# Kernel optimization log

Hardware: AMD Instinct MI355X
Metric: run time of the kernel (lower is better)

## Reference

```python
import jax, jax.numpy as jnp
import numpy as np

B, S, E, H = 4, 2048, 1024, 8
D = E // H  # head_dim = 128


def setup_inputs() -> dict:
    key = jax.random.key(0)
    ks = jax.random.split(key, 7)
    scale = 1.0 / np.sqrt(D)
    return {
        "sequences": jax.random.normal(ks[0], (B, S, E), dtype=jnp.float32),
        # per-head Linear weights, torch layout [out, in] stacked over heads
        "Wq": jax.random.normal(ks[1], (H, D, D), dtype=jnp.float32) * scale,
        "Wk": jax.random.normal(ks[2], (H, D, D), dtype=jnp.float32) * scale,
        "Wv": jax.random.normal(ks[3], (H, D, D), dtype=jnp.float32) * scale,
        "bq": jax.random.normal(ks[4], (H, D), dtype=jnp.float32) * scale,
        "bk": jax.random.normal(ks[5], (H, D), dtype=jnp.float32) * scale,
        "bv": jax.random.normal(ks[6], (H, D), dtype=jnp.float32) * scale,
    }


def reference(sequences, Wq, Wk, Wv, bq, bk, bv):
    # split feature dim into heads: [B,S,H,D]
    xh = sequences.reshape(B, S, H, D)
    # torch Linear: y = x @ W.T + b  ->  contract input dim d with W[h, o, d]
    q = jnp.einsum("bshd,hod->bsho", xh, Wq) + bq
    k = jnp.einsum("bshd,hod->bsho", xh, Wk) + bk
    v = jnp.einsum("bshd,hod->bsho", xh, Wv) + bv
    # NOTE: original scales by 1/sqrt(num_heads), not 1/sqrt(head_dim)
    scores = jnp.einsum("bshd,bthd->bhst", q, k) / jnp.sqrt(jnp.float32(H))
    attn = jax.nn.softmax(scores, axis=-1)  # [B,H,S,S]
    out = jnp.einsum("bhst,bthd->bshd", attn, v)
    # hstack over heads == reshape back to [B,S,E]
    return out.reshape(B, S, E)
```

## Files before the change

kernel.cpp:

```cpp
#include <hip/hip_runtime.h>
#include <hip/hip_bf16.h>

#define B_ 4
#define S_ 2048
#define E_ 1024
#define H_ 8
#define D_ 128

using f16x8 = __attribute__((ext_vector_type(8))) _Float16;
using f32x4 = __attribute__((ext_vector_type(4))) float;

__device__ __forceinline__ ushort f2h_bits(float f) {
    union { _Float16 h; ushort u; } cv; cv.h = (_Float16)f; return cv.u;
}
__device__ __forceinline__ f16x8 pack8(const float* __restrict__ p) {
    float4 f0 = *(const float4*)p;
    float4 f1 = *(const float4*)(p + 4);
    f16x8 r;
    r[0] = (_Float16)f0.x; r[1] = (_Float16)f0.y;
    r[2] = (_Float16)f0.z; r[3] = (_Float16)f0.w;
    r[4] = (_Float16)f1.x; r[5] = (_Float16)f1.y;
    r[6] = (_Float16)f1.z; r[7] = (_Float16)f1.w;
    return r;
}

__global__ __launch_bounds__(256) void kv_proj(
    const float* __restrict__ seq,
    const float* __restrict__ Wk, const float* __restrict__ Wv,
    const float* __restrict__ bk, const float* __restrict__ bv,
    ushort* __restrict__ ko, ushort* __restrict__ vo)
{
    constexpr int TS = 136;
    __shared__ ushort Tk[128 * TS];
    __shared__ ushort Tv[128 * TS];
    const int m0 = blockIdx.x * 128, h = blockIdx.y;
    const int tid = threadIdx.x, lane = tid & 63, w = tid >> 6;
    const int l16 = lane & 15, quad = lane >> 4;

    f16x8 a[2][4];
    #pragma unroll
    for (int mt = 0; mt < 2; ++mt)
        #pragma unroll
        for (int ks = 0; ks < 4; ++ks)
            a[mt][ks] = pack8(&seq[(size_t)(m0 + w * 32 + mt * 16 + l16) * E_
                                   + h * D_ + ks * 32 + quad * 8]);

    {
        const float* W = Wk + (size_t)h * D_ * D_;
        f32x4 acc[2][8];
        #pragma unroll
        for (int mt = 0; mt < 2; ++mt)
            #pragma unroll
            for (int nt = 0; nt < 8; ++nt) { f32x4 z = {0.f,0.f,0.f,0.f}; acc[mt][nt] = z; }
        #pragma unroll
        for (int ks = 0; ks < 4; ++ks)
            #pragma unroll
            for (int nt = 0; nt < 8; ++nt) {
                f16x8 bfr = pack8(&W[(size_t)(nt * 16 + l16) * D_ + ks * 32 + quad * 8]);
                #pragma unroll
                for (int mt = 0; mt < 2; ++mt)
                    acc[mt][nt] = __builtin_amdgcn_mfma_f32_16x16x32_f16(
                        a[mt][ks], bfr, acc[mt][nt], 0, 0, 0);
            }
        #pragma unroll
        for (int nt = 0; nt < 8; ++nt) {
            int o = nt * 16 + l16;
            float bias = bk[h * D_ + o];
            #pragma unroll
            for (int mt = 0; mt < 2; ++mt)
                #pragma unroll
                for (int r = 0; r < 4; ++r) {
                    int row = w * 32 + mt * 16 + quad * 4 + r;
                    Tk[row * TS + (o ^ (quad << 3))] = f2h_bits(acc[mt][nt][r] + bias);
                }
        }
    }
    {
        const float* W = Wv + (size_t)h * D_ * D_;
        f32x4 acc[2][8];
        #pragma unroll
        for (int mt = 0; mt < 2; ++mt)
            #pragma unroll
            for (int nt = 0; nt < 8; ++nt) { f32x4 z = {0.f,0.f,0.f,0.f}; acc[mt][nt] = z; }
        #pragma unroll
        for (int ks = 0; ks < 4; ++ks)
            #pragma unroll
            for (int nt = 0; nt < 8; ++nt) {
                f16x8 bfr = pack8(&W[(size_t)(nt * 16 + l16) * D_ + ks * 32 + quad * 8]);
                #pragma unroll
                for (int mt = 0; mt < 2; ++mt)
                    acc[mt][nt] = __builtin_amdgcn_mfma_f32_16x16x32_f16(
                        a[mt][ks], bfr, acc[mt][nt], 0, 0, 0);
            }
        #pragma unroll
        for (int nt = 0; nt < 8; ++nt) {
            int o = nt * 16 + l16;
            float bias = bv[h * D_ + o];
            #pragma unroll
            for (int mt = 0; mt < 2; ++mt)
                #pragma unroll
                for (int r = 0; r < 4; ++r) {
                    int row = w * 32 + mt * 16 + quad * 4 + r;
                    Tv[o * TS + row] = f2h_bits(acc[mt][nt][r] + bias);
                }
        }
    }
    __syncthreads();

    #pragma unroll
    for (int i = 0; i < 8; ++i) {
        int idx = tid + i * 256;
        int row = idx >> 4, c8 = (idx & 15) * 8;
        uint4 dk = *(uint4*)&Tk[row * TS + (c8 ^ (((row >> 2) & 3) << 3))];
        int m = m0 + row, bi = m >> 11, s = m & (S_ - 1);
        *(uint4*)&ko[(((size_t)bi * H_ + h) * S_ + s) * D_ + c8] = dk;
        uint4 dv = *(uint4*)&Tv[row * TS + c8];
        int mg = m0 + c8, bv_i = mg >> 11, s0 = mg & (S_ - 1);
        *(uint4*)&vo[(((size_t)bv_i * H_ + h) * D_ + row) * S_ + s0] = dv;
    }
}

__global__ __launch_bounds__(256) void attn(
    const float* __restrict__ seq, const float* __restrict__ Wq,
    const float* __restrict__ bq,
    const ushort* __restrict__ kg, const ushort* __restrict__ vtg,
    float* __restrict__ out)
{
    constexpr int KS = 136;
    constexpr int VS = 136;
    __shared__ alignas(16) ushort smem[128 * KS + 128 * VS];
    ushort* const Klds = smem;
    ushort* const Vt   = smem + 128 * KS;

    const int m0 = blockIdx.x * 128;
    const int h = blockIdx.y, bi = blockIdx.z;
    const int bh = bi * H_ + h;
    const int tid = threadIdx.x, lane = tid & 63, w = tid >> 6;
    const int l16 = lane & 15, quad = lane >> 4;
    const size_t baseK = (size_t)bh * S_ * D_;
    const size_t baseV = (size_t)bh * D_ * S_;
    const float qscale = 0.35355339059327373f * 1.4426950408889634f;
    const int qq_r = (l16 >> 2) & 3;

    {
        f16x8 xa[2][4];
        #pragma unroll
        for (int mt = 0; mt < 2; ++mt)
            #pragma unroll
            for (int ks = 0; ks < 4; ++ks)
                xa[mt][ks] = pack8(&seq[((size_t)bi * S_ + m0 + w * 32 + mt * 16 + l16) * E_
                                        + h * D_ + ks * 32 + quad * 8]);
        f32x4 qacc[2][8];
        #pragma unroll
        for (int mt = 0; mt < 2; ++mt)
            #pragma unroll
            for (int nt = 0; nt < 8; ++nt) { f32x4 z = {0.f,0.f,0.f,0.f}; qacc[mt][nt] = z; }
        const float* W = Wq + (size_t)h * D_ * D_;
        #pragma unroll
        for (int ks = 0; ks < 4; ++ks)
            #pragma unroll
            for (int nt = 0; nt < 8; ++nt) {
                f16x8 bfr = pack8(&W[(size_t)(nt * 16 + l16) * D_ + ks * 32 + quad * 8]);
                #pragma unroll
                for (int mt = 0; mt < 2; ++mt)
                    qacc[mt][nt] = __builtin_amdgcn_mfma_f32_16x16x32_f16(
                        xa[mt][ks], bfr, qacc[mt][nt], 0, 0, 0);
            }
        #pragma unroll
        for (int nt = 0; nt < 8; ++nt) {
            int o = nt * 16 + l16;
            float bias = bq[h * D_ + o];
            #pragma unroll
            for (int mt = 0; mt < 2; ++mt)
                #pragma unroll
                for (int r = 0; r < 4; ++r) {
                    int row = w * 32 + mt * 16 + quad * 4 + r;
                    Klds[row * KS + (o ^ (quad << 3))] =
                        f2h_bits((qacc[mt][nt][r] + bias) * qscale);
                }
        }
    }
    __syncthreads();

    f16x8 qf[2][4];
    #pragma unroll
    for (int mt = 0; mt < 2; ++mt)
        #pragma unroll
        for (int ks = 0; ks < 4; ++ks)
            qf[mt][ks] = *(const f16x8*)&Klds[(w * 32 + mt * 16 + l16) * KS
                                              + ks * 32 + ((quad ^ qq_r) << 3)];

    f32x4 o_acc[2][8];
    #pragma unroll
    for (int mt = 0; mt < 2; ++mt)
        #pragma unroll
        for (int nt = 0; nt < 8; ++nt) { f32x4 z = {0.f,0.f,0.f,0.f}; o_acc[mt][nt] = z; }
    float m_prev[2] = {-1e30f, -1e30f};
    float l_lane[2] = {0.f, 0.f};

    for (int j = 0; j < S_ / 128; ++j) {
        const int n0 = j * 128;
        __syncthreads();
        #pragma unroll
        for (int i = 0; i < 8; ++i) {
            int idx = tid + i * 256;
            int r = idx >> 4, c8 = (idx & 15) * 8;
            *(uint4*)&Klds[r * KS + c8] =
                *(const uint4*)&kg[baseK + (size_t)(n0 + r) * D_ + c8];
        }
        #pragma unroll
        for (int i = 0; i < 8; ++i) {
            int idx = tid + i * 256;
            int d = idx >> 4, c8 = (idx & 15) * 8;
            *(uint4*)&Vt[d * VS + c8] =
                *(const uint4*)&vtg[baseV + (size_t)d * S_ + n0 + c8];
        }
        __syncthreads();

        f32x4 sacc[2][8];
        #pragma unroll
        for (int mt = 0; mt < 2; ++mt)
            #pragma unroll
            for (int nt = 0; nt < 8; ++nt) { f32x4 z = {0.f,0.f,0.f,0.f}; sacc[mt][nt] = z; }
        __builtin_amdgcn_s_setprio(1);
        #pragma unroll
        for (int ks = 0; ks < 4; ++ks)
            #pragma unroll
            for (int nt = 0; nt < 8; ++nt) {
                f16x8 kf = *(const f16x8*)&Klds[(nt * 16 + l16) * KS + ks * 32 + quad * 8];
                #pragma unroll
                for (int mt = 0; mt < 2; ++mt)
                    sacc[mt][nt] = __builtin_amdgcn_mfma_f32_16x16x32_f16(
                        kf, qf[mt][ks], sacc[mt][nt], 0, 0, 0);
            }
        __builtin_amdgcn_s_setprio(0);

        uint2 pkw[2][8];
        #pragma unroll
        for (int mt = 0; mt < 2; ++mt) {
            float mx4[8];
            #pragma unroll
            for (int nt = 0; nt < 8; ++nt)
                mx4[nt] = fmaxf(fmaxf(sacc[mt][nt][0], sacc[mt][nt][1]),
                                fmaxf(sacc[mt][nt][2], sacc[mt][nt][3]));
            float mx = fmaxf(fmaxf(fmaxf(mx4[0], mx4[1]), fmaxf(mx4[2], mx4[3])),
                             fmaxf(fmaxf(mx4[4], mx4[5]), fmaxf(mx4[6], mx4[7])));
            mx = fmaxf(mx, __shfl_xor(mx, 16));
            mx = fmaxf(mx, __shfl_xor(mx, 32));
            if (__any(mx > m_prev[mt] + 8.0f)) {
                float mnew  = fmaxf(m_prev[mt], mx);
                float alpha = exp2f(m_prev[mt] - mnew);
                #pragma unroll
                for (int nt = 0; nt < 8; ++nt)
                    #pragma unroll
                    for (int r = 0; r < 4; ++r) o_acc[mt][nt][r] *= alpha;
                l_lane[mt] *= alpha;
                m_prev[mt] = mnew;
            }
            #pragma unroll
            for (int nt = 0; nt < 8; ++nt) {
                float e0 = exp2f(sacc[mt][nt][0] - m_prev[mt]);
                float e1 = exp2f(sacc[mt][nt][1] - m_prev[mt]);
                float e2 = exp2f(sacc[mt][nt][2] - m_prev[mt]);
                float e3 = exp2f(sacc[mt][nt][3] - m_prev[mt]);
                auto p01 = __builtin_amdgcn_cvt_pkrtz(e0, e1);
                auto p23 = __builtin_amdgcn_cvt_pkrtz(e2, e3);
                l_lane[mt] += (float)p01[0] + (float)p01[1]
                            + (float)p23[0] + (float)p23[1];
                pkw[mt][nt] = make_uint2(__builtin_bit_cast(uint, p01),
                                         __builtin_bit_cast(uint, p23));
            }
        }

        __syncthreads();
        #pragma unroll
        for (int mt = 0; mt < 2; ++mt) {
            const int qrow = w * 32 + mt * 16 + l16;
            #pragma unroll
            for (int nt = 0; nt < 8; ++nt)
                *(uint2*)&Klds[qrow * KS + nt * 16 + quad * 4] = pkw[mt][nt];
        }

        __builtin_amdgcn_s_setprio(1);
        #pragma unroll
        for (int ks = 0; ks < 4; ++ks) {
            f16x8 pb[2];
            #pragma unroll
            for (int mt = 0; mt < 2; ++mt)
                pb[mt] = *(const f16x8*)&Klds[(w * 32 + mt * 16 + l16) * KS
                                              + ks * 32 + quad * 8];
            #pragma unroll
            for (int nt = 0; nt < 8; ++nt) {
                f16x8 vf = *(const f16x8*)&Vt[(nt * 16 + l16) * VS + ks * 32 + quad * 8];
                #pragma unroll
                for (int mt = 0; mt < 2; ++mt)
                    o_acc[mt][nt] = __builtin_amdgcn_mfma_f32_16x16x32_f16(
                        vf, pb[mt], o_acc[mt][nt], 0, 0, 0);
            }
        }
        __builtin_amdgcn_s_setprio(0);
    }

    #pragma unroll
    for (int mt = 0; mt < 2; ++mt) {
        float l = l_lane[mt];
        l += __shfl_xor(l, 16);
        l += __shfl_xor(l, 32);
        float rinv = 1.0f / l;
        const int q = m0 + w * 32 + mt * 16 + l16;
        #pragma unroll
        for (int nt = 0; nt < 8; ++nt) {
            float4 o;
            o.x = o_acc[mt][nt][0] * rinv;
            o.y = o_acc[mt][nt][1] * rinv;
            o.z = o_acc[mt][nt][2] * rinv;
            o.w = o_acc[mt][nt][3] * rinv;
            *(float4*)&out[((size_t)bi * S_ + q) * E_ + h * D_ + nt * 16 + quad * 4] = o;
        }
    }
}

extern "C" void kernel_launch(void* const* d_in, const int* in_sizes, int n_in,
                              void* d_out, int out_size, void* d_ws, size_t ws_size,
                              hipStream_t stream) {
    const float* seq = (const float*)d_in[0];
    const float* Wq  = (const float*)d_in[1];
    const float* Wk  = (const float*)d_in[2];
    const float* Wv  = (const float*)d_in[3];
    const float* bq  = (const float*)d_in[4];
    const float* bk  = (const float*)d_in[5];
    const float* bv  = (const float*)d_in[6];

    const size_t per = (size_t)B_ * H_ * S_ * D_;
    if (ws_size < 2 * per * sizeof(ushort)) return;
    ushort* kws  = (ushort*)d_ws;
    ushort* vtws = kws + per;

    kv_proj<<<dim3(B_ * S_ / 128, H_), 256, 0, stream>>>(
        seq, Wk, Wv, bk, bv, kws, vtws);
    attn<<<dim3(S_ / 128, H_, B_), 256, 0, stream>>>(
        seq, Wq, bq, kws, vtws, (float*)d_out);
}
```

Measured before the change: 293.8 us.

## Double-buffer K/V with direct global-to-LDS loads and 512-thread attention blocks

The attention kernel moves to 8 waves per block, with each wave owning 16 query rows instead of 32. K and V tiles are now fetched with global_load_lds DMA into double-buffered LDS, so the next tile's load overlaps the current tile's compute, and each loop iteration needs only one barrier. An XOR swizzle, applied in kv_proj's stores and matched in the attention reads, replaces the padded row strides to avoid bank conflicts. The trade-off is heavy LDS use (about 160 KB), which likely limits residency to one block per CU where two could run before.

```diff
diff --git a/kernel.cpp b/kernel.cpp
--- a/kernel.cpp
+++ b/kernel.cpp
@@ -22,6 +22,12 @@
     r[4] = (_Float16)f1.x; r[5] = (_Float16)f1.y;
     r[6] = (_Float16)f1.z; r[7] = (_Float16)f1.w;
     return r;
+}
+
+__device__ __forceinline__ void gll16(const ushort* g, ushort* l) {
+    __builtin_amdgcn_global_load_lds(
+        (const __attribute__((address_space(1))) unsigned int*)g,
+        (__attribute__((address_space(3))) unsigned int*)l, 16, 0, 0);
 }
 
 __global__ __launch_bounds__(256) void kv_proj(
@@ -111,210 +117,193 @@
     for (int i = 0; i < 8; ++i) {
         int idx = tid + i * 256;
         int row = idx >> 4, c8 = (idx & 15) * 8;
-        uint4 dk = *(uint4*)&Tk[row * TS + (c8 ^ (((row >> 2) & 3) << 3))];
+        int lk = c8 ^ ((row & 7) << 3);
+        uint4 dk = *(uint4*)&Tk[row * TS + (lk ^ (((row >> 2) & 3) << 3))];
         int m = m0 + row, bi = m >> 11, s = m & (S_ - 1);
         *(uint4*)&ko[(((size_t)bi * H_ + h) * S_ + s) * D_ + c8] = dk;
-        uint4 dv = *(uint4*)&Tv[row * TS + c8];
+        uint4 dv = *(uint4*)&Tv[row * TS + (c8 ^ ((row & 7) << 3))];
         int mg = m0 + c8, bv_i = mg >> 11, s0 = mg & (S_ - 1);
         *(uint4*)&vo[(((size_t)bv_i * H_ + h) * D_ + row) * S_ + s0] = dv;
     }
 }
 
-__global__ __launch_bounds__(256) void attn(
+__global__ __launch_bounds__(512) void attn(
     const float* __restrict__ seq, const float* __restrict__ Wq,
     const float* __restrict__ bq,
     const ushort* __restrict__ kg, const ushort* __restrict__ vtg,
     float* __restrict__ out)
 {
-    constexpr int KS = 136;
-    constexpr int VS = 136;
-    __shared__ alignas(16) ushort smem[128 * KS + 128 * VS];
-    ushort* const Klds = smem;
-    ushort* const Vt   = smem + 128 * KS;
+    __shared__ alignas(16) ushort Kbuf[2][128 * 128];
+    __shared__ alignas(16) ushort Vbuf[2][128 * 128];
+    __shared__ alignas(16) ushort Pbuf[128 * 128];
 
     const int m0 = blockIdx.x * 128;
     const int h = blockIdx.y, bi = blockIdx.z;
     const int bh = bi * H_ + h;
     const int tid = threadIdx.x, lane = tid & 63, w = tid >> 6;
     const int l16 = lane & 15, quad = lane >> 4;
-    const size_t baseK = (size_t)bh * S_ * D_;
-    const size_t baseV = (size_t)bh * D_ * S_;
+    const ushort* kbase = kg + (size_t)bh * S_ * D_;
+    const ushort* vbase = vtg + (size_t)bh * D_ * S_;
     const float qscale = 0.35355339059327373f * 1.4426950408889634f;
-    const int qq_r = (l16 >> 2) & 3;
+
+    #pragma unroll
+    for (int i = 0; i < 4; ++i) {
+        int b = i * 8 + w;
+        gll16(kbase + (size_t)b * 512 + lane * 8, &Kbuf[0][0] + b * 512);
+        gll16(vbase + (size_t)(b * 4 + (lane >> 4)) * S_ + (lane & 15) * 8,
+              &Vbuf[0][0] + b * 512);
+    }
 
     {
-        f16x8 xa[2][4];
-        #pragma unroll
-        for (int mt = 0; mt < 2; ++mt)
-            #pragma unroll
-            for (int ks = 0; ks < 4; ++ks)
-                xa[mt][ks] = pack8(&seq[((size_t)bi * S_ + m0 + w * 32 + mt * 16 + l16) * E_
-                                        + h * D_ + ks * 32 + quad * 8]);
-        f32x4 qacc[2][8];
-        #pragma unroll
-        for (int mt = 0; mt < 2; ++mt)
-            #pragma unroll
-            for (int nt = 0; nt < 8; ++nt) { f32x4 z = {0.f,0.f,0.f,0.f}; qacc[mt][nt] = z; }
+        f16x8 xa[4];
+        #pragma unroll
+        for (int ks = 0; ks < 4; ++ks)
+            xa[ks] = pack8(&seq[((size_t)bi * S_ + m0 + w * 16 + l16) * E_
+                                + h * D_ + ks * 32 + quad * 8]);
+        f32x4 qacc[8];
+        #pragma unroll
+        for (int nt = 0; nt < 8; ++nt) { f32x4 z = {0.f,0.f,0.f,0.f}; qacc[nt] = z; }
         const float* W = Wq + (size_t)h * D_ * D_;
         #pragma unroll
         for (int ks = 0; ks < 4; ++ks)
             #pragma unroll
             for (int nt = 0; nt < 8; ++nt) {
                 f16x8 bfr = pack8(&W[(size_t)(nt * 16 + l16) * D_ + ks * 32 + quad * 8]);
-                #pragma unroll
-                for (int mt = 0; mt < 2; ++mt)
-                    qacc[mt][nt] = __builtin_amdgcn_mfma_f32_16x16x32_f16(
-                        xa[mt][ks], bfr, qacc[mt][nt], 0, 0, 0);
+                qacc[nt] = __builtin_amdgcn_mfma_f32_16x16x32_f16(
+                    xa[ks], bfr, qacc[nt], 0, 0, 0);
             }
         #pragma unroll
         for (int nt = 0; nt < 8; ++nt) {
             int o = nt * 16 + l16;
             float bias = bq[h * D_ + o];
             #pragma unroll
-            for (int mt = 0; mt < 2; ++mt)
-                #pragma unroll
-                for (int r = 0; r < 4; ++r) {
-                    int row = w * 32 + mt * 16 + quad * 4 + r;
-                    Klds[row * KS + (o ^ (quad << 3))] =
-                        f2h_bits((qacc[mt][nt][r] + bias) * qscale);
-                }
-        }
-    }
+            for (int r = 0; r < 4; ++r) {
+                int row = w * 16 + quad * 4 + r;
+                Pbuf[row * 128 + (o ^ (quad << 3))] =
+                    f2h_bits((qacc[nt][r] + bias) * qscale);
+            }
+        }
+    }
+    f16x8 qf[4];
+    #pragma unroll
+    for (int ks = 0; ks < 4; ++ks)
+        qf[ks] = *(const f16x8*)&Pbuf[(w * 16 + l16) * 128
+                                      + ks * 32 + ((quad ^ (l16 >> 2)) << 3)];
+
+    f32x4 o_acc[8];
+    #pragma unroll
+    for (int nt = 0; nt < 8; ++nt) { f32x4 z = {0.f,0.f,0.f,0.f}; o_acc[nt] = z; }
+    float m_prev = -1e30f, l_lane = 0.f;
+
     __syncthreads();
 
-    f16x8 qf[2][4];
-    #pragma unroll
-    for (int mt = 0; mt < 2; ++mt)
-        #pragma unroll
-        for (int ks = 0; ks < 4; ++ks)
-            qf[mt][ks] = *(const f16x8*)&Klds[(w * 32 + mt * 16 + l16) * KS
-                                              + ks * 32 + ((quad ^ qq_r) << 3)];
-
-    f32x4 o_acc[2][8];
-    #pragma unroll
-    for (int mt = 0; mt < 2; ++mt)
-        #pragma unroll
-        for (int nt = 0; nt < 8; ++nt) { f32x4 z = {0.f,0.f,0.f,0.f}; o_acc[mt][nt] = z; }
-    float m_prev[2] = {-1e30f, -1e30f};
-    float l_lane[2] = {0.f, 0.f};
+    const int psw = (l16 & 7) << 1;
+    const int kvsw = l16 & 7;
 
     for (int j = 0; j < S_ / 128; ++j) {
-        const int n0 = j * 128;
-        __syncthreads();
-        #pragma unroll
-        for (int i = 0; i < 8; ++i) {
-            int idx = tid + i * 256;
-            int r = idx >> 4, c8 = (idx & 15) * 8;
-            *(uint4*)&Klds[r * KS + c8] =
-                *(const uint4*)&kg[baseK + (size_t)(n0 + r) * D_ + c8];
-        }
-        #pragma unroll
-        for (int i = 0; i < 8; ++i) {
-            int idx = tid + i * 256;
-            int d = idx >> 4, c8 = (idx & 15) * 8;
-            *(uint4*)&Vt[d * VS + c8] =
-                *(const uint4*)&vtg[baseV + (size_t)d * S_ + n0 + c8];
-        }
-        __syncthreads();
-
-        f32x4 sacc[2][8];
-        #pragma unroll
-        for (int mt = 0; mt < 2; ++mt)
-            #pragma unroll
-            for (int nt = 0; nt < 8; ++nt) { f32x4 z = {0.f,0.f,0.f,0.f}; sacc[mt][nt] = z; }
+        const int cur = j & 1;
+        const ushort* KL = &Kbuf[cur][0];
+        const ushort* VL = &Vbuf[cur][0];
+
+        if (j + 1 < S_ / 128) {
+            const int n1 = (j + 1) * 128;
+            const ushort* kt = kbase + (size_t)n1 * D_;
+            const ushort* vt = vbase + n1;
+            ushort* kd = &Kbuf[cur ^ 1][0];
+            ushort* vd = &Vbuf[cur ^ 1][0];
+            #pragma unroll
+            for (int i = 0; i < 4; ++i) {
+                int b = i * 8 + w;
+                gll16(kt + (size_t)b * 512 + lane * 8, kd + b * 512);
+                gll16(vt + (size_t)(b * 4 + (lane >> 4)) * S_ + (lane & 15) * 8,
+                      vd + b * 512);
+            }
+        }
+
+        f32x4 sacc[8];
+        #pragma unroll
+        for (int nt = 0; nt < 8; ++nt) { f32x4 z = {0.f,0.f,0.f,0.f}; sacc[nt] = z; }
         __builtin_amdgcn_s_setprio(1);
         #pragma unroll
         for (int ks = 0; ks < 4; ++ks)
             #pragma unroll
             for (int nt = 0; nt < 8; ++nt) {
-                f16x8 kf = *(const f16x8*)&Klds[(nt * 16 + l16) * KS + ks * 32 + quad * 8];
-                #pragma unroll
-                for (int mt = 0; mt < 2; ++mt)
-                    sacc[mt][nt] = __builtin_amdgcn_mfma_f32_16x16x32_f16(
-                        kf, qf[mt][ks], sacc[mt][nt], 0, 0, 0);
+                f16x8 kf = *(const f16x8*)&KL[(nt * 16 + l16) * 128
+                                              + (((ks * 4 + quad) ^ kvsw) << 3)];
+                sacc[nt] = __builtin_amdgcn_mfma_f32_16x16x32_f16(
+                    kf, qf[ks], sacc[nt], 0, 0, 0);
             }
         __builtin_amdgcn_s_setprio(0);
 
-        uint2 pkw[2][8];
-        #pragma unroll
-        for (int mt = 0; mt < 2; ++mt) {
-            float mx4[8];
-            #pragma unroll
-            for (int nt = 0; nt < 8; ++nt)
-                mx4[nt] = fmaxf(fmaxf(sacc[mt][nt][0], sacc[mt][nt][1]),
-                                fmaxf(sacc[mt][nt][2], sacc[mt][nt][3]));
-            float mx = fmaxf(fmaxf(fmaxf(mx4[0], mx4[1]), fmaxf(mx4[2], mx4[3])),
-                             fmaxf(fmaxf(mx4[4], mx4[5]), fmaxf(mx4[6], mx4[7])));
+        uint2 pkw[8];
+        {
+            float mx = fmaxf(fmaxf(sacc[0][0], sacc[0][1]), fmaxf(sacc[0][2], sacc[0][3]));
+            #pragma unroll
+            for (int nt = 1; nt < 8; ++nt)
+                mx = fmaxf(mx, fmaxf(fmaxf(sacc[nt][0], sacc[nt][1]),
+                                     fmaxf(sacc[nt][2], sacc[nt][3])));
             mx = fmaxf(mx, __shfl_xor(mx, 16));
             mx = fmaxf(mx, __shfl_xor(mx, 32));
-            if (__any(mx > m_prev[mt] + 8.0f)) {
-                float mnew  = fmaxf(m_prev[mt], mx);
-                float alpha = exp2f(m_prev[mt] - mnew);
+            if (__any(mx > m_prev + 8.0f)) {
+                float mnew  = fmaxf(m_prev, mx);
+                float alpha = exp2f(m_prev - mnew);
                 #pragma unroll
                 for (int nt = 0; nt < 8; ++nt)
                     #pragma unroll
-                    for (int r = 0; r < 4; ++r) o_acc[mt][nt][r] *= alpha;
-                l_lane[mt] *= alpha;
-                m_prev[mt] = mnew;
-            }
-            #pragma unroll
-            for (int nt = 0; nt < 8; ++nt) {
-                float e0 = exp2f(sacc[mt][nt][0] - m_prev[mt]);
-                float e1 = exp2f(sacc[mt][nt][1] - m_prev[mt]);
-                float e2 = exp2f(sacc[mt][nt][2] - m_prev[mt]);
-                float e3 = exp2f(sacc[mt][nt][3] - m_prev[mt]);
+                    for (int r = 0; r < 4; ++r) o_acc[nt][r] *= alpha;
+                l_lane *= alpha;
+                m_prev = mnew;
+            }
+            #pragma unroll
+            for (int nt = 0; nt < 8; ++nt) {
+                float e0 = exp2f(sacc[nt][0] - m_prev);
+                float e1 = exp2f(sacc[nt][1] - m_prev);
+                float e2 = exp2f(sacc[nt][2] - m_prev);
+                float e3 = exp2f(sacc[nt][3] - m_prev);
                 auto p01 = __builtin_amdgcn_cvt_pkrtz(e0, e1);
                 auto p23 = __builtin_amdgcn_cvt_pkrtz(e2, e3);
-                l_lane[mt] += (float)p01[0] + (float)p01[1]
-                            + (float)p23[0] + (float)p23[1];
-                pkw[mt][nt] = make_uint2(__builtin_bit_cast(uint, p01),
-                                         __builtin_bit_cast(uint, p23));
-            }
-        }
+                l_lane += (float)p01[0] + (float)p01[1] + (float)p23[0] + (float)p23[1];
+                pkw[nt] = make_uint2(__builtin_bit_cast(uint, p01),
+                                     __builtin_bit_cast(uint, p23));
+            }
+        }
+
+        const int qrow = w * 16 + l16;
+        ushort* prow = &Pbuf[qrow * 128];
+        #pragma unroll
+        for (int nt = 0; nt < 8; ++nt)
+            *(uint2*)&prow[((nt * 4 + quad) ^ psw) << 2] = pkw[nt];
+
+        __builtin_amdgcn_s_setprio(1);
+        #pragma unroll
+        for (int ks = 0; ks < 4; ++ks) {
+            f16x8 pb = *(const f16x8*)&prow[((ks * 8 + quad * 2) ^ psw) << 2];
+            #pragma unroll
+            for (int nt = 0; nt < 8; ++nt) {
+                f16x8 vf = *(const f16x8*)&VL[(nt * 16 + l16) * 128
+                                              + (((ks * 4 + quad) ^ kvsw) << 3)];
+                o_acc[nt] = __builtin_amdgcn_mfma_f32_16x16x32_f16(
+                    vf, pb, o_acc[nt], 0, 0, 0);
+            }
+        }
+        __builtin_amdgcn_s_setprio(0);
 
         __syncthreads();
-        #pragma unroll
-        for (int mt = 0; mt < 2; ++mt) {
-            const int qrow = w * 32 + mt * 16 + l16;
-            #pragma unroll
-            for (int nt = 0; nt < 8; ++nt)
-                *(uint2*)&Klds[qrow * KS + nt * 16 + quad * 4] = pkw[mt][nt];
-        }
-
-        __builtin_amdgcn_s_setprio(1);
-        #pragma unroll
-        for (int ks = 0; ks < 4; ++ks) {
-            f16x8 pb[2];
-            #pragma unroll
-            for (int mt = 0; mt < 2; ++mt)
-                pb[mt] = *(const f16x8*)&Klds[(w * 32 + mt * 16 + l16) * KS
-                                              + ks * 32 + quad * 8];
-            #pragma unroll
-            for (int nt = 0; nt < 8; ++nt) {
-                f16x8 vf = *(const f16x8*)&Vt[(nt * 16 + l16) * VS + ks * 32 + quad * 8];
-                #pragma unroll
-                for (int mt = 0; mt < 2; ++mt)
-                    o_acc[mt][nt] = __builtin_amdgcn_mfma_f32_16x16x32_f16(
-                        vf, pb[mt], o_acc[mt][nt], 0, 0, 0);
-            }
-        }
-        __builtin_amdgcn_s_setprio(0);
-    }
-
-    #pragma unroll
-    for (int mt = 0; mt < 2; ++mt) {
-        float l = l_lane[mt];
+    }
+
+    {
+        float l = l_lane;
         l += __shfl_xor(l, 16);
         l += __shfl_xor(l, 32);
         float rinv = 1.0f / l;
-        const int q = m0 + w * 32 + mt * 16 + l16;
+        const int q = m0 + w * 16 + l16;
         #pragma unroll
         for (int nt = 0; nt < 8; ++nt) {
             float4 o;
-            o.x = o_acc[mt][nt][0] * rinv;
-            o.y = o_acc[mt][nt][1] * rinv;
-            o.z = o_acc[mt][nt][2] * rinv;
-            o.w = o_acc[mt][nt][3] * rinv;
+            o.x = o_acc[nt][0] * rinv;
+            o.y = o_acc[nt][1] * rinv;
+            o.z = o_acc[nt][2] * rinv;
+            o.w = o_acc[nt][3] * rinv;
             *(float4*)&out[((size_t)bi * S_ + q) * E_ + h * D_ + nt * 16 + quad * 4] = o;
         }
     }
@@ -338,6 +327,6 @@
 
     kv_proj<<<dim3(B_ * S_ / 128, H_), 256, 0, stream>>>(
         seq, Wk, Wv, bk, bv, kws, vtws);
-    attn<<<dim3(S_ / 128, H_, B_), 256, 0, stream>>>(
+    attn<<<dim3(S_ / 128, H_, B_), 512, 0, stream>>>(
         seq, Wq, bq, kws, vtws, (float*)d_out);
 }
```

Result: faster. 279.6 us (-4.8%).

## Double-buffer K/V tiles with async global_load_lds and XOR-swizzled LDS

Applied to the files above, without the earlier changes.

Replaces the synchronous per-iteration K/V copy through registers with direct global-to-LDS async loads into double buffers, prefetching the next 64-key tile while the current one is computed. The KV tile shrinks from 128 to 64 keys, and the LDS layout switches from padded rows to XOR swizzling. kv_proj is changed to emit K and V already pre-swizzled to match. This aims to hide global load latency and remove one barrier per iteration, at the cost of more iterations and more reliance on exact swizzle and synchronisation correctness.

```diff
diff --git a/kernel.cpp b/kernel.cpp
--- a/kernel.cpp
+++ b/kernel.cpp
@@ -22,6 +22,12 @@
     r[4] = (_Float16)f1.x; r[5] = (_Float16)f1.y;
     r[6] = (_Float16)f1.z; r[7] = (_Float16)f1.w;
     return r;
+}
+
+__device__ __forceinline__ void gll16(const ushort* g, ushort* l) {
+    __builtin_amdgcn_global_load_lds(
+        (const __attribute__((address_space(1))) unsigned int*)g,
+        (__attribute__((address_space(3))) unsigned int*)l, 16, 0, 0);
 }
 
 __global__ __launch_bounds__(256) void kv_proj(
@@ -111,10 +117,11 @@
     for (int i = 0; i < 8; ++i) {
         int idx = tid + i * 256;
         int row = idx >> 4, c8 = (idx & 15) * 8;
-        uint4 dk = *(uint4*)&Tk[row * TS + (c8 ^ (((row >> 2) & 3) << 3))];
+        int lk = c8 ^ ((row & 7) << 3);
+        uint4 dk = *(uint4*)&Tk[row * TS + (lk ^ (((row >> 2) & 3) << 3))];
         int m = m0 + row, bi = m >> 11, s = m & (S_ - 1);
         *(uint4*)&ko[(((size_t)bi * H_ + h) * S_ + s) * D_ + c8] = dk;
-        uint4 dv = *(uint4*)&Tv[row * TS + c8];
+        uint4 dv = *(uint4*)&Tv[row * TS + (c8 ^ ((row & 7) << 3))];
         int mg = m0 + c8, bv_i = mg >> 11, s0 = mg & (S_ - 1);
         *(uint4*)&vo[(((size_t)bv_i * H_ + h) * D_ + row) * S_ + s0] = dv;
     }
@@ -126,22 +133,31 @@
     const ushort* __restrict__ kg, const ushort* __restrict__ vtg,
     float* __restrict__ out)
 {
-    constexpr int KS = 136;
-    constexpr int VS = 136;
-    __shared__ alignas(16) ushort smem[128 * KS + 128 * VS];
-    ushort* const Klds = smem;
-    ushort* const Vt   = smem + 128 * KS;
+    constexpr int NT = S_ / 64;
+    __shared__ alignas(16) ushort Kbuf[2][64 * 128];
+    __shared__ alignas(16) ushort Vbuf[2][128 * 64];
+    __shared__ alignas(16) ushort Pbuf[128 * 64];
 
     const int m0 = blockIdx.x * 128;
     const int h = blockIdx.y, bi = blockIdx.z;
     const int bh = bi * H_ + h;
     const int tid = threadIdx.x, lane = tid & 63, w = tid >> 6;
     const int l16 = lane & 15, quad = lane >> 4;
-    const size_t baseK = (size_t)bh * S_ * D_;
-    const size_t baseV = (size_t)bh * D_ * S_;
+    const int swz = l16 & 7;
+    const ushort* kbase = kg + (size_t)bh * S_ * D_;
+    const ushort* vbase = vtg + (size_t)bh * D_ * S_;
     const float qscale = 0.35355339059327373f * 1.4426950408889634f;
-    const int qq_r = (l16 >> 2) & 3;
-
+
+    #pragma unroll
+    for (int c = 0; c < 4; ++c) {
+        int i = w * 4 + c;
+        gll16(kbase + i * 512 + lane * 8, &Kbuf[0][0] + i * 512);
+        gll16(vbase + (size_t)(i * 8 + (lane >> 3)) * S_ + (lane & 7) * 8,
+              &Vbuf[0][0] + i * 512);
+    }
+
+    ushort* const Qs = (w < 2) ? &Pbuf[0] : &Kbuf[1][0];
+    const int qlr = (w & 1) * 32;
     {
         f16x8 xa[2][4];
         #pragma unroll
@@ -174,21 +190,19 @@
             for (int mt = 0; mt < 2; ++mt)
                 #pragma unroll
                 for (int r = 0; r < 4; ++r) {
-                    int row = w * 32 + mt * 16 + quad * 4 + r;
-                    Klds[row * KS + (o ^ (quad << 3))] =
+                    int row = qlr + mt * 16 + quad * 4 + r;
+                    Qs[row * 128 + (o ^ (quad << 3))] =
                         f2h_bits((qacc[mt][nt][r] + bias) * qscale);
                 }
         }
     }
-    __syncthreads();
-
     f16x8 qf[2][4];
     #pragma unroll
     for (int mt = 0; mt < 2; ++mt)
         #pragma unroll
         for (int ks = 0; ks < 4; ++ks)
-            qf[mt][ks] = *(const f16x8*)&Klds[(w * 32 + mt * 16 + l16) * KS
-                                              + ks * 32 + ((quad ^ qq_r) << 3)];
+            qf[mt][ks] = *(const f16x8*)&Qs[(qlr + mt * 16 + l16) * 128
+                                            + ks * 32 + ((quad ^ (l16 >> 2)) << 3)];
 
     f32x4 o_acc[2][8];
     #pragma unroll
@@ -198,36 +212,39 @@
     float m_prev[2] = {-1e30f, -1e30f};
     float l_lane[2] = {0.f, 0.f};
 
-    for (int j = 0; j < S_ / 128; ++j) {
-        const int n0 = j * 128;
-        __syncthreads();
-        #pragma unroll
-        for (int i = 0; i < 8; ++i) {
-            int idx = tid + i * 256;
-            int r = idx >> 4, c8 = (idx & 15) * 8;
-            *(uint4*)&Klds[r * KS + c8] =
-                *(const uint4*)&kg[baseK + (size_t)(n0 + r) * D_ + c8];
-        }
-        #pragma unroll
-        for (int i = 0; i < 8; ++i) {
-            int idx = tid + i * 256;
-            int d = idx >> 4, c8 = (idx & 15) * 8;
-            *(uint4*)&Vt[d * VS + c8] =
-                *(const uint4*)&vtg[baseV + (size_t)d * S_ + n0 + c8];
-        }
-        __syncthreads();
-
-        f32x4 sacc[2][8];
-        #pragma unroll
-        for (int mt = 0; mt < 2; ++mt)
-            #pragma unroll
-            for (int nt = 0; nt < 8; ++nt) { f32x4 z = {0.f,0.f,0.f,0.f}; sacc[mt][nt] = z; }
+    __syncthreads();
+
+    for (int j = 0; j < NT; ++j) {
+        const int cur = j & 1;
+        const ushort* KL = &Kbuf[cur][0];
+        const ushort* VL = &Vbuf[cur][0];
+
+        if (j + 1 < NT) {
+            const ushort* kt = kbase + (size_t)(j + 1) * 64 * 128;
+            const ushort* vt = vbase + (j + 1) * 64;
+            ushort* kd = &Kbuf[cur ^ 1][0];
+            ushort* vd = &Vbuf[cur ^ 1][0];
+            #pragma unroll
+            for (int c = 0; c < 4; ++c) {
+                int i = w * 4 + c;
+                gll16(kt + i * 512 + lane * 8, kd + i * 512);
+                gll16(vt + (size_t)(i * 8 + (lane >> 3)) * S_ + (lane & 7) * 8,
+                      vd + i * 512);
+            }
+        }
+
+        f32x4 sacc[2][4];
+        #pragma unroll
+        for (int mt = 0; mt < 2; ++mt)
+            #pragma unroll
+            for (int nt = 0; nt < 4; ++nt) { f32x4 z = {0.f,0.f,0.f,0.f}; sacc[mt][nt] = z; }
         __builtin_amdgcn_s_setprio(1);
         #pragma unroll
         for (int ks = 0; ks < 4; ++ks)
             #pragma unroll
-            for (int nt = 0; nt < 8; ++nt) {
-                f16x8 kf = *(const f16x8*)&Klds[(nt * 16 + l16) * KS + ks * 32 + quad * 8];
+            for (int nt = 0; nt < 4; ++nt) {
+                f16x8 kf = *(const f16x8*)&KL[(nt * 16 + l16) * 128
+                                              + (((ks * 4 + quad) ^ swz) << 3)];
                 #pragma unroll
                 for (int mt = 0; mt < 2; ++mt)
                     sacc[mt][nt] = __builtin_amdgcn_mfma_f32_16x16x32_f16(
@@ -235,16 +252,15 @@
             }
         __builtin_amdgcn_s_setprio(0);
 
-        uint2 pkw[2][8];
+        uint2 pkw[2][4];
         #pragma unroll
         for (int mt = 0; mt < 2; ++mt) {
-            float mx4[8];
-            #pragma unroll
-            for (int nt = 0; nt < 8; ++nt)
-                mx4[nt] = fmaxf(fmaxf(sacc[mt][nt][0], sacc[mt][nt][1]),
-                                fmaxf(sacc[mt][nt][2], sacc[mt][nt][3]));
-            float mx = fmaxf(fmaxf(fmaxf(mx4[0], mx4[1]), fmaxf(mx4[2], mx4[3])),
-                             fmaxf(fmaxf(mx4[4], mx4[5]), fmaxf(mx4[6], mx4[7])));
+            float mx = fmaxf(fmaxf(sacc[mt][0][0], sacc[mt][0][1]),
+                             fmaxf(sacc[mt][0][2], sacc[mt][0][3]));
+            #pragma unroll
+            for (int nt = 1; nt < 4; ++nt)
+                mx = fmaxf(mx, fmaxf(fmaxf(sacc[mt][nt][0], sacc[mt][nt][1]),
+                                     fmaxf(sacc[mt][nt][2], sacc[mt][nt][3])));
             mx = fmaxf(mx, __shfl_xor(mx, 16));
             mx = fmaxf(mx, __shfl_xor(mx, 32));
             if (__any(mx > m_prev[mt] + 8.0f)) {
@@ -258,7 +274,7 @@
                 m_prev[mt] = mnew;
             }
             #pragma unroll
-            for (int nt = 0; nt < 8; ++nt) {
+            for (int nt = 0; nt < 4; ++nt) {
                 float e0 = exp2f(sacc[mt][nt][0] - m_prev[mt]);
                 float e1 = exp2f(sacc[mt][nt][1] - m_prev[mt]);
                 float e2 = exp2f(sacc[mt][nt][2] - m_prev[mt]);
@@ -272,26 +288,28 @@
             }
         }
 
-        __syncthreads();
         #pragma unroll
         for (int mt = 0; mt < 2; ++mt) {
-            const int qrow = w * 32 + mt * 16 + l16;
-            #pragma unroll
-            for (int nt = 0; nt < 8; ++nt)
-                *(uint2*)&Klds[qrow * KS + nt * 16 + quad * 4] = pkw[mt][nt];
+            ushort* prow = &Pbuf[(w * 32 + mt * 16 + l16) * 64];
+            #pragma unroll
+            for (int nt = 0; nt < 4; ++nt) {
+                int G = 2 * nt + (quad >> 1);
+                *(uint2*)&prow[((G ^ swz) << 3) + ((quad & 1) << 2)] = pkw[mt][nt];
+            }
         }
 
         __builtin_amdgcn_s_setprio(1);
         #pragma unroll
-        for (int ks = 0; ks < 4; ++ks) {
+        for (int ks = 0; ks < 2; ++ks) {
             f16x8 pb[2];
             #pragma unroll
             for (int mt = 0; mt < 2; ++mt)
-                pb[mt] = *(const f16x8*)&Klds[(w * 32 + mt * 16 + l16) * KS
-                                              + ks * 32 + quad * 8];
+                pb[mt] = *(const f16x8*)&Pbuf[(w * 32 + mt * 16 + l16) * 64
+                                              + (((ks * 4 + quad) ^ swz) << 3)];
             #pragma unroll
             for (int nt = 0; nt < 8; ++nt) {
-                f16x8 vf = *(const f16x8*)&Vt[(nt * 16 + l16) * VS + ks * 32 + quad * 8];
+                f16x8 vf = *(const f16x8*)&VL[(nt * 16 + l16) * 64
+                                              + (((ks * 4 + quad) ^ swz) << 3)];
                 #pragma unroll
                 for (int mt = 0; mt < 2; ++mt)
                     o_acc[mt][nt] = __builtin_amdgcn_mfma_f32_16x16x32_f16(
@@ -299,6 +317,8 @@
             }
         }
         __builtin_amdgcn_s_setprio(0);
+
+        __syncthreads();
     }
 
     #pragma unroll
```

New measurement: 304.7 us. 3.7% more time.
